# Kernel tuning notes

Hardware: AMD Instinct MI355X
Metric: run time of the kernel (lower is better)

Reference implementation:

```python
import jax, jax.numpy as jnp
import numpy as np


def setup_inputs() -> dict:
    key = jax.random.key(0)
    ks = jax.random.split(key, 7)
    B, T, E, H = 4, 4096, 1024, 64
    return {
        "idx": jax.random.normal(ks[0], (B, T, E), dtype=jnp.float32),
        "Wq": jax.random.normal(ks[1], (E, H), dtype=jnp.float32) * (E ** -0.5),
        "bq": jax.random.normal(ks[2], (H,), dtype=jnp.float32) * 0.01,
        "Wk": jax.random.normal(ks[3], (E, H), dtype=jnp.float32) * (E ** -0.5),
        "bk": jax.random.normal(ks[4], (H,), dtype=jnp.float32) * 0.01,
        "Wv": jax.random.normal(ks[5], (E, H), dtype=jnp.float32) * (E ** -0.5),
        "bv": jax.random.normal(ks[6], (H,), dtype=jnp.float32) * 0.01,
    }


def reference(idx, Wq, bq, Wk, bk, Wv, bv):
    # idx: [B, T, E]
    d = idx.shape[-1]  # note: torch code scales by n_embd**-0.5, NOT head_size
    Q = idx @ Wq + bq  # [B, T, H]
    K = idx @ Wk + bk
    V = idx @ Wv + bv
    # scores; NOTE: original torch code calls wei.masked_fill(...) non-in-place
    # and discards the result, so no causal mask is applied. No softmax either.
    wei = jnp.einsum("bth,bsh->bts", Q, K) * (d ** -0.5)  # [B, T, T]
    out = jnp.einsum("bts,bsh->bth", wei, V)  # [B, T, H]
    return out
```

## Files before the change

### kernel.cpp

```cpp
#include <hip/hip_runtime.h>


typedef __attribute__((ext_vector_type(8))) short bf16x8;
typedef __attribute__((ext_vector_type(4))) float f32x4;

#define MFMA16(a, b, c) __builtin_amdgcn_mfma_f32_16x16x32_bf16((a), (b), (c), 0, 0, 0)

__device__ __forceinline__ unsigned short f2bf(float f) {
    unsigned int u = __float_as_uint(f);
    u += 0x7fffu + ((u >> 16) & 1u);
    return (unsigned short)(u >> 16);
}

__device__ __forceinline__ void load_lds16(const float* g, float* l) {
    __builtin_amdgcn_global_load_lds(
        (const __attribute__((address_space(1))) unsigned int*)g,
        (__attribute__((address_space(3))) unsigned int*)l, 16, 0, 0);
}

__global__ void prep(const float* __restrict__ Wq, const float* __restrict__ Wk,
                     const float* __restrict__ Wv, unsigned short* __restrict__ WB) {
    int t = blockIdx.x * 256 + threadIdx.x;
    int k0i = t / 768;
    int rem = t - k0i * 768;
    int nt = rem >> 6, lane = rem & 63;
    int n = nt * 16 + (lane & 15);
    int kb = k0i * 32 + ((lane >> 4) * 8);
    int mm = n >> 6, h = n & 63;
    const float* W = (mm == 0) ? Wq : (mm == 1) ? Wk : Wv;
    float sc = (mm == 1) ? 0.03125f : 1.0f;
    bf16x8 v;
    #pragma unroll
    for (int j = 0; j < 8; j++) v[j] = (short)f2bf(W[(size_t)(kb + j) * 64 + h] * sc);
    *(bf16x8*)(WB + (size_t)t * 8) = v;
}

__global__ __launch_bounds__(256, 2) void qkv(
    const float* __restrict__ idx, const unsigned short* __restrict__ WB,
    const float* __restrict__ bq, const float* __restrict__ bk, const float* __restrict__ bv,
    unsigned short* __restrict__ Q, unsigned short* __restrict__ Kt,
    unsigned short* __restrict__ Vt) {
    __shared__ float As[2][32][260];
    const int lane = threadIdx.x & 63, w = threadIdx.x >> 6;
    const int r0 = blockIdx.x * 32;

    auto stage_load = [&](int s, int buf) {
        #pragma unroll
        for (int i = 0; i < 8; i++) {
            int r = i * 4 + w;
            const float* g = idx + (size_t)(r0 + r) * 1024 + s * 256 + lane * 4;
            load_lds16(g, &As[buf][r][0]);
        }
    };

    const f32x4 z4 = {0.f, 0.f, 0.f, 0.f};
    f32x4 acc[2][3];
    #pragma unroll
    for (int mt = 0; mt < 2; mt++)
        #pragma unroll
        for (int j = 0; j < 3; j++) acc[mt][j] = z4;

    stage_load(0, 0);
    for (int s = 0; s < 4; s++) {
        __syncthreads();
        if (s < 3) stage_load(s + 1, (s + 1) & 1);
        const int buf = s & 1;
        #pragma unroll
        for (int kk = 0; kk < 8; kk++) {
            bf16x8 aF[2];
            #pragma unroll
            for (int mt = 0; mt < 2; mt++) {
                const float* ap = &As[buf][mt * 16 + (lane & 15)][kk * 32 + (lane >> 4) * 8];
                float4 lo = *(const float4*)ap;
                float4 hi = *(const float4*)(ap + 4);
                bf16x8 a;
                a[0] = (short)f2bf(lo.x); a[1] = (short)f2bf(lo.y);
                a[2] = (short)f2bf(lo.z); a[3] = (short)f2bf(lo.w);
                a[4] = (short)f2bf(hi.x); a[5] = (short)f2bf(hi.y);
                a[6] = (short)f2bf(hi.z); a[7] = (short)f2bf(hi.w);
                aF[mt] = a;
            }
            const unsigned short* Bp = WB + (size_t)(((s * 8 + kk) * 12) * 64 + lane) * 8;
            #pragma unroll
            for (int j = 0; j < 3; j++) {
                int nt = w + j * 4;
                bf16x8 bb = *(const bf16x8*)(Bp + nt * 512);
                acc[0][j] = MFMA16(aF[0], bb, acc[0][j]);
                acc[1][j] = MFMA16(aF[1], bb, acc[1][j]);
            }
        }
    }

    const int h = w * 16 + (lane & 15);
    #pragma unroll
    for (int j = 0; j < 3; j++) {
        float bias = (j == 0) ? bq[h] : (j == 1) ? bk[h] * 0.03125f : bv[h];
        #pragma unroll
        for (int mt = 0; mt < 2; mt++) {
            int rbase = r0 + mt * 16 + (lane >> 4) * 4;
            #pragma unroll
            for (int reg = 0; reg < 4; reg++) {
                int r = rbase + reg;
                unsigned short v = f2bf(acc[mt][j][reg] + bias);
                if (j == 0) {
                    Q[(size_t)r * 64 + h] = v;
                } else {
                    int b = r >> 12, t = r & 4095;
                    unsigned short* dst = (j == 1) ? Kt : Vt;
                    dst[(size_t)b * 262144 + h * 4096 + t] = v;
                }
            }
        }
    }
}

__global__ __launch_bounds__(256) void ktv_partial(
    const unsigned short* __restrict__ Kt, const unsigned short* __restrict__ Vt,
    float* __restrict__ part) {
    const int lane = threadIdx.x & 63, wave = threadIdx.x >> 6;
    const int c = blockIdx.x, b = blockIdx.y;
    const unsigned short* Kb = Kt + (size_t)b * 262144;
    const unsigned short* Vb = Vt + (size_t)b * 262144;
    const f32x4 z4 = {0.f, 0.f, 0.f, 0.f};
    f32x4 acc[4] = {z4, z4, z4, z4};
    const int m  = 16 * wave + (lane & 15);
    const int tq = (lane >> 4) * 8;
    #pragma unroll
    for (int it = 0; it < 4; it++) {
        int t0 = c * 128 + it * 32 + tq;
        bf16x8 a = *(const bf16x8*)&Kb[(size_t)m * 4096 + t0];
        #pragma unroll
        for (int nt = 0; nt < 4; nt++) {
            bf16x8 bb = *(const bf16x8*)&Vb[(size_t)(nt * 16 + (lane & 15)) * 4096 + t0];
            acc[nt] = MFMA16(a, bb, acc[nt]);
        }
    }
    float* P = part + (size_t)(b * 32 + c) * 4096;
    const int rowb = 16 * wave + (lane >> 4) * 4;
    #pragma unroll
    for (int nt = 0; nt < 4; nt++)
        #pragma unroll
        for (int reg = 0; reg < 4; reg++)
            P[(rowb + reg) * 64 + nt * 16 + (lane & 15)] = acc[nt][reg];
}

__global__ void reduce_m(const float* __restrict__ part,
                         unsigned short* __restrict__ Mt) {
    int i = blockIdx.x * 256 + threadIdx.x;
    int b = i >> 12, h1 = (i >> 6) & 63, h2 = i & 63;
    float s = 0.f;
    #pragma unroll
    for (int cc = 0; cc < 32; cc++)
        s += part[(size_t)(b * 32 + cc) * 4096 + h1 * 64 + h2];
    Mt[(size_t)b * 4096 + h2 * 64 + h1] = f2bf(s);
}

__global__ __launch_bounds__(256) void qm(
    const unsigned short* __restrict__ Q, const unsigned short* __restrict__ Mt,
    float* __restrict__ out) {
    const int lane = threadIdx.x & 63, wave = threadIdx.x >> 6;
    const int r0 = blockIdx.x * 64;
    const int b  = r0 >> 12;
    const f32x4 z4 = {0.f, 0.f, 0.f, 0.f};
    f32x4 acc[4] = {z4, z4, z4, z4};
    const int rr = r0 + 16 * wave + (lane & 15);
    const int kq = (lane >> 4) * 8;
    #pragma unroll
    for (int ks = 0; ks < 2; ks++) {
        int k0 = ks * 32;
        bf16x8 a = *(const bf16x8*)&Q[(size_t)rr * 64 + k0 + kq];
        #pragma unroll
        for (int nt = 0; nt < 4; nt++) {
            bf16x8 bb = *(const bf16x8*)&Mt[(size_t)b * 4096 + (nt * 16 + (lane & 15)) * 64 + k0 + kq];
            acc[nt] = MFMA16(a, bb, acc[nt]);
        }
    }
    const int rowb = r0 + 16 * wave + (lane >> 4) * 4;
    #pragma unroll
    for (int nt = 0; nt < 4; nt++)
        #pragma unroll
        for (int reg = 0; reg < 4; reg++)
            out[(size_t)(rowb + reg) * 64 + nt * 16 + (lane & 15)] = acc[nt][reg];
}

extern "C" void kernel_launch(void* const* d_in, const int* in_sizes, int n_in,
                              void* d_out, int out_size, void* d_ws, size_t ws_size,
                              hipStream_t stream) {
    const float* idx = (const float*)d_in[0];
    const float* Wq  = (const float*)d_in[1];
    const float* bq  = (const float*)d_in[2];
    const float* Wk  = (const float*)d_in[3];
    const float* bk  = (const float*)d_in[4];
    const float* Wv  = (const float*)d_in[5];
    const float* bv  = (const float*)d_in[6];
    float* out = (float*)d_out;

    char* ws = (char*)d_ws;
    unsigned short* WB = (unsigned short*)(ws);
    float*          Pp = (float*)(ws);
    unsigned short* Q  = (unsigned short*)(ws + (2048u << 10));
    unsigned short* Kt = (unsigned short*)(ws + (4096u << 10));
    unsigned short* Vt = (unsigned short*)(ws + (6144u << 10));
    unsigned short* Mt = (unsigned short*)(ws + (8192u << 10));

    hipLaunchKernelGGL(prep,        dim3(96),     dim3(256), 0, stream, Wq, Wk, Wv, WB);
    hipLaunchKernelGGL(qkv,         dim3(512),    dim3(256), 0, stream,
                       idx, WB, bq, bk, bv, Q, Kt, Vt);
    hipLaunchKernelGGL(ktv_partial, dim3(32, 4),  dim3(256), 0, stream, Kt, Vt, Pp);
    hipLaunchKernelGGL(reduce_m,    dim3(64),     dim3(256), 0, stream, Pp, Mt);
    hipLaunchKernelGGL(qm,          dim3(256),    dim3(256), 0, stream, Q, Mt, out);
}
```

Baseline: 129.7 us.

## Convert activation tile to bf16 once in LDS instead of per-MFMA conversion

The qkv kernel now loads the whole 32x1024 fp32 input tile through registers, converts it to bf16 once, and stores it in padded LDS. The previous double-buffered async global-to-LDS pipeline and its repeated per-wave fp32-to-bf16 conversion are removed. This halves LDS traffic and drops redundant conversions across the four waves. In exchange, global loads no longer overlap with MFMA compute, since everything is loaded before a single barrier.

```diff
diff --git a/kernel.cpp b/kernel.cpp
--- a/kernel.cpp
+++ b/kernel.cpp
@@ -12,20 +12,14 @@
     return (unsigned short)(u >> 16);
 }
 
-__device__ __forceinline__ void load_lds16(const float* g, float* l) {
-    __builtin_amdgcn_global_load_lds(
-        (const __attribute__((address_space(1))) unsigned int*)g,
-        (__attribute__((address_space(3))) unsigned int*)l, 16, 0, 0);
-}
-
 __global__ void prep(const float* __restrict__ Wq, const float* __restrict__ Wk,
                      const float* __restrict__ Wv, unsigned short* __restrict__ WB) {
     int t = blockIdx.x * 256 + threadIdx.x;
-    int k0i = t / 768;
-    int rem = t - k0i * 768;
+    int kki = t / 768;
+    int rem = t - kki * 768;
     int nt = rem >> 6, lane = rem & 63;
     int n = nt * 16 + (lane & 15);
-    int kb = k0i * 32 + ((lane >> 4) * 8);
+    int kb = kki * 32 + ((lane >> 4) * 8);
     int mm = n >> 6, h = n & 63;
     const float* W = (mm == 0) ? Wq : (mm == 1) ? Wk : Wv;
     float sc = (mm == 1) ? 0.03125f : 1.0f;
@@ -40,18 +34,29 @@
     const float* __restrict__ bq, const float* __restrict__ bk, const float* __restrict__ bv,
     unsigned short* __restrict__ Q, unsigned short* __restrict__ Kt,
     unsigned short* __restrict__ Vt) {
-    __shared__ float As[2][32][260];
+    __shared__ unsigned short As[32 * 1032];
     const int lane = threadIdx.x & 63, w = threadIdx.x >> 6;
     const int r0 = blockIdx.x * 32;
 
-    auto stage_load = [&](int s, int buf) {
-        #pragma unroll
-        for (int i = 0; i < 8; i++) {
-            int r = i * 4 + w;
-            const float* g = idx + (size_t)(r0 + r) * 1024 + s * 256 + lane * 4;
-            load_lds16(g, &As[buf][r][0]);
-        }
-    };
+    const float* src = idx + (size_t)(r0 + w * 8) * 1024;
+    #pragma unroll
+    for (int batch = 0; batch < 4; batch++) {
+        float4 v[8];
+        #pragma unroll
+        for (int j = 0; j < 8; j++)
+            v[j] = *(const float4*)(src + (size_t)(batch * 8 + j) * 256 + lane * 4);
+        #pragma unroll
+        for (int j = 0; j < 8; j++) {
+            int i   = batch * 8 + j;
+            int row = w * 8 + (i >> 2);
+            int k   = (i & 3) * 256 + lane * 4;
+            unsigned int lo = ((unsigned int)f2bf(v[j].y) << 16) | f2bf(v[j].x);
+            unsigned int hi = ((unsigned int)f2bf(v[j].w) << 16) | f2bf(v[j].z);
+            uint2 p; p.x = lo; p.y = hi;
+            *(uint2*)(As + (size_t)row * 1032 + k) = p;
+        }
+    }
+    __syncthreads();
 
     const f32x4 z4 = {0.f, 0.f, 0.f, 0.f};
     f32x4 acc[2][3];
@@ -60,34 +65,19 @@
         #pragma unroll
         for (int j = 0; j < 3; j++) acc[mt][j] = z4;
 
-    stage_load(0, 0);
-    for (int s = 0; s < 4; s++) {
-        __syncthreads();
-        if (s < 3) stage_load(s + 1, (s + 1) & 1);
-        const int buf = s & 1;
-        #pragma unroll
-        for (int kk = 0; kk < 8; kk++) {
-            bf16x8 aF[2];
-            #pragma unroll
-            for (int mt = 0; mt < 2; mt++) {
-                const float* ap = &As[buf][mt * 16 + (lane & 15)][kk * 32 + (lane >> 4) * 8];
-                float4 lo = *(const float4*)ap;
-                float4 hi = *(const float4*)(ap + 4);
-                bf16x8 a;
-                a[0] = (short)f2bf(lo.x); a[1] = (short)f2bf(lo.y);
-                a[2] = (short)f2bf(lo.z); a[3] = (short)f2bf(lo.w);
-                a[4] = (short)f2bf(hi.x); a[5] = (short)f2bf(hi.y);
-                a[6] = (short)f2bf(hi.z); a[7] = (short)f2bf(hi.w);
-                aF[mt] = a;
-            }
-            const unsigned short* Bp = WB + (size_t)(((s * 8 + kk) * 12) * 64 + lane) * 8;
-            #pragma unroll
-            for (int j = 0; j < 3; j++) {
-                int nt = w + j * 4;
-                bf16x8 bb = *(const bf16x8*)(Bp + nt * 512);
-                acc[0][j] = MFMA16(aF[0], bb, acc[0][j]);
-                acc[1][j] = MFMA16(aF[1], bb, acc[1][j]);
-            }
+    const int al = lane & 15;
+    const int kq = (lane >> 4) * 8;
+    #pragma unroll 4
+    for (int kk = 0; kk < 32; kk++) {
+        bf16x8 a0 = *(const bf16x8*)(As + (size_t)al * 1032 + kk * 32 + kq);
+        bf16x8 a1 = *(const bf16x8*)(As + (size_t)(16 + al) * 1032 + kk * 32 + kq);
+        const unsigned short* Bp = WB + (size_t)((kk * 12) * 64 + lane) * 8;
+        #pragma unroll
+        for (int j = 0; j < 3; j++) {
+            int nt = w + j * 4;
+            bf16x8 bb = *(const bf16x8*)(Bp + nt * 512);
+            acc[0][j] = MFMA16(a0, bb, acc[0][j]);
+            acc[1][j] = MFMA16(a1, bb, acc[1][j]);
         }
     }
 
```

Result: no change. 128.2 us (-1.1%).
